# Kernel tuning notes

Measured on AMD Instinct MI355X. Metric: run time of the kernel, lower is better.

Reference implementation:

```python
import jax, jax.numpy as jnp
import numpy as np

N_POWER_SERIES = 8  # 'fixed' estimator, n_power_series=8, n_samples=4 (leading axis of v)


def _g_fn(x, W1, b1, W2, b2):
    # residual branch g(x): Linear -> ELU -> Linear (canonical i-ResNet block)
    return jax.nn.elu(x @ W1 + b1) @ W2 + b2


def setup_inputs() -> dict:
    key = jax.random.key(0)
    ks = jax.random.split(key, 4)
    B, D, H, S = 8192, 1024, 4096, 4
    x = jax.random.normal(ks[0], (B, D), jnp.float32)
    # scale weights so g is roughly contractive (Lipschitz < 1), as spectral norm enforces
    W1 = jax.random.normal(ks[1], (D, H), jnp.float32) * (0.5 / np.sqrt(D))
    b1 = jnp.zeros((H,), jnp.float32)
    W2 = jax.random.normal(ks[2], (H, D), jnp.float32) * (0.5 / np.sqrt(H))
    b2 = jnp.zeros((D,), jnp.float32)
    v = jax.random.normal(ks[3], (S, B, D), jnp.float32)  # Hutchinson probes
    log_df_dz = jnp.zeros((B,), jnp.float32)
    return {"x": x, "log_df_dz": log_df_dz, "W1": W1, "b1": b1, "W2": W2, "b2": b2, "v": v}


def reference(x, log_df_dz, W1, b1, W2, b2, v):
    g, vjp_fn = jax.vjp(lambda xx: _g_fn(xx, W1, b1, W2, b2), x)
    vjp = lambda w: vjp_fn(w)[0]  # w^T J, w: [B, D]

    w = v                      # [S, B, D]
    sum_diag = jnp.zeros(v.shape[:2], v.dtype)  # [S, B]
    for k in range(1, N_POWER_SERIES + 1):
        w = jax.vmap(vjp)(w)                        # v^T J^k
        inner = jnp.einsum('sbd,sbd->sb', w, v)     # Hutchinson tr(J^k) estimate
        sign = 1.0 if (k % 2 == 1) else -1.0
        sum_diag = sum_diag + sign * (inner / k)
    logdet = jnp.mean(sum_diag, axis=0)             # mean over samples -> [B]

    z = x + g
    return z, log_df_dz + logdet
```

## Files before the change

kernel.cpp:

```cpp
#include <hip/hip_runtime.h>
#include <hip/hip_bf16.h>

using bf16 = __hip_bfloat16;
typedef __attribute__((ext_vector_type(8))) short bf16x8;
typedef __attribute__((ext_vector_type(4))) float f32x4;

__device__ __forceinline__ float b2f(unsigned short u) {
  union { unsigned int i; float f; } x; x.i = ((unsigned int)u) << 16; return x.f;
}
__device__ __forceinline__ unsigned short f2b(float f) {
  __hip_bfloat16 h = __float2bfloat16(f);
  return *reinterpret_cast<unsigned short*>(&h);
}

__device__ __forceinline__ void load16_to_lds(const bf16* g, void* lds) {
  __builtin_amdgcn_global_load_lds((const __attribute__((address_space(1))) void*)g,
                                   (__attribute__((address_space(3))) void*)lds, 16, 0, 0);
}

#define FENCE() asm volatile("" ::: "memory")
#define BAR() do { FENCE(); __builtin_amdgcn_s_barrier(); FENCE(); } while (0)
#define SCHED_PIN() __builtin_amdgcn_sched_barrier(0)

__global__ void cast_f32_bf16(const float* __restrict__ in, bf16* __restrict__ out, size_t n) {
  size_t i0 = ((size_t)blockIdx.x * 256 + threadIdx.x) * 4;
  size_t stride = (size_t)gridDim.x * 256 * 4;
  for (size_t i = i0; i < n; i += stride) {
    float4 f = *(const float4*)(in + i);
    ushort4 o;
    o.x = f2b(f.x); o.y = f2b(f.y); o.z = f2b(f.z); o.w = f2b(f.w);
    *(ushort4*)(out + i) = o;
  }
}

__global__ void transpose_cast(const float* __restrict__ in, bf16* __restrict__ out, int R, int C) {
  __shared__ float tile[32][33];
  int tx = threadIdx.x & 31, ty = threadIdx.x >> 5;
  int r0 = blockIdx.y * 32, c0 = blockIdx.x * 32;
  #pragma unroll
  for (int i = 0; i < 32; i += 8)
    tile[ty + i][tx] = in[(size_t)(r0 + ty + i) * C + (c0 + tx)];
  __syncthreads();
  #pragma unroll
  for (int i = 0; i < 32; i += 8)
    out[(size_t)(c0 + ty + i) * R + (r0 + tx)] = __float2bfloat16(tile[tx][ty + i]);
}

template<int EPI>
__global__ __launch_bounds__(512, 2)
void gemm256(const bf16* __restrict__ A, const bf16* __restrict__ Bm,
             int M, int N, int K,
             bf16* __restrict__ OutB,
             const float* __restrict__ bias,
             const bf16* __restrict__ Ea) {
  __shared__ __align__(16) char pool[131072];
  char* Albs = pool;
  char* Blbs = pool + 65536;
  const int tid = threadIdx.x;
  const int l = tid & 63, w = tid >> 6;
  const int lane16 = l & 15, lh = l >> 4;
  const int wr = w >> 2, wc = w & 3;
  const int bm0 = blockIdx.y * 256, bn0 = blockIdx.x * 256;
  const int NT2 = K >> 7;

  auto stage = [&](const bf16* G, int grow0, int kbase, char* ldsbase) {
    #pragma unroll
    for (int r = 0; r < 2; ++r) {
      int p = (r * 512 + tid) * 16;
      int row = p >> 7, colb = p & 127;
      int cs = colb ^ ((row & 7) << 4);
      const bf16* g = G + (size_t)(grow0 + row) * K + kbase + (cs >> 1);
      load16_to_lds(g, ldsbase + (size_t)(r * 512 + w * 64) * 16);
    }
  };
  auto rd = [&](const char* base, int row, int colb) -> bf16x8 {
    return *(const bf16x8*)(base + row * 128 + (colb ^ ((row & 7) << 4)));
  };

  f32x4 acc[8][4] = {};
  bf16x8 a_r[4][2], b_r[4][2];

  #define RD_A(mq, buf) { _Pragma("unroll") for (int i = 0; i < 4; ++i) \
      _Pragma("unroll") for (int kk = 0; kk < 2; ++kk) \
      a_r[i][kk] = rd(Albs + (buf) * 32768, wr * 128 + (mq) * 64 + i * 16 + lane16, kk * 64 + lh * 16); }
  #define RD_B(buf) { _Pragma("unroll") for (int nf = 0; nf < 4; ++nf) \
      _Pragma("unroll") for (int kk = 0; kk < 2; ++kk) \
      b_r[nf][kk] = rd(Blbs + (buf) * 32768, wc * 64 + nf * 16 + lane16, kk * 64 + lh * 16); }
  #define MFMA_H(mq, n0) { __builtin_amdgcn_s_setprio(1); \
      _Pragma("unroll") for (int i = 0; i < 4; ++i) \
      _Pragma("unroll") for (int nn = 0; nn < 2; ++nn) \
      _Pragma("unroll") for (int kk = 0; kk < 2; ++kk) \
        acc[(mq)*4+i][(n0)+nn] = __builtin_amdgcn_mfma_f32_16x16x32_bf16( \
            a_r[i][kk], b_r[(n0)+nn][kk], acc[(mq)*4+i][(n0)+nn], 0, 0, 0); \
      __builtin_amdgcn_s_setprio(0); }
  #define PHASE(BODY_PRE, MFMA_CALL) { BODY_PRE; BAR(); SCHED_PIN(); MFMA_CALL; SCHED_PIN(); BAR(); }

  stage(Bm, bn0 + 0,   0,  Blbs + 0);
  stage(Bm, bn0 + 128, 0,  Blbs + 16384);
  stage(A,  bm0 + 0,   0,  Albs + 0);
  stage(A,  bm0 + 128, 0,  Albs + 16384);
  stage(Bm, bn0 + 0,   64, Blbs + 32768);
  stage(Bm, bn0 + 128, 64, Blbs + 32768 + 16384);
  stage(A,  bm0 + 0,   64, Albs + 32768);
  asm volatile("s_waitcnt vmcnt(6)" ::: "memory");
  SCHED_PIN();
  BAR();

  for (int t = 0; t < NT2; ++t) {
    const int k2 = (2 * t + 2) * 64, k3 = (2 * t + 3) * 64;
    const bool nl = (t < NT2 - 1);
    PHASE({ RD_B(0); RD_A(0, 0); stage(A, bm0 + 128, (2 * t + 1) * 64, Albs + 32768 + 16384); },
          MFMA_H(0, 0));
    PHASE({ if (nl) stage(Bm, bn0 + 0, k2, Blbs + 0); }, MFMA_H(0, 2));
    PHASE({ RD_A(1, 0); if (nl) stage(Bm, bn0 + 128, k2, Blbs + 16384); }, MFMA_H(1, 0));
    { if (nl) stage(A, bm0 + 0, k2, Albs + 0);
      BAR(); SCHED_PIN(); MFMA_H(1, 2); SCHED_PIN();
      if (nl) { asm volatile("s_waitcnt vmcnt(6)" ::: "memory"); }
      else    { asm volatile("s_waitcnt vmcnt(0)" ::: "memory"); }
      SCHED_PIN(); BAR(); }
    PHASE({ RD_B(1); RD_A(0, 1); if (nl) stage(A, bm0 + 128, k2, Albs + 16384); },
          MFMA_H(0, 0));
    PHASE({ if (nl) stage(Bm, bn0 + 0, k3, Blbs + 32768); }, MFMA_H(0, 2));
    PHASE({ RD_A(1, 1); if (nl) stage(Bm, bn0 + 128, k3, Blbs + 32768 + 16384); }, MFMA_H(1, 0));
    { if (nl) stage(A, bm0 + 0, k3, Albs + 32768);
      BAR(); SCHED_PIN(); MFMA_H(1, 2); SCHED_PIN();
      if (nl) { asm volatile("s_waitcnt vmcnt(6)" ::: "memory"); }
      SCHED_PIN(); BAR(); }
  }

  float* scr = (float*)(pool + w * 4352);
  const int row0 = bm0 + wr * 128, col0 = bn0 + wc * 64;
  const int erow = l >> 3, ecol = (l & 7) * 8;
  f32x4 bias0 = {}, bias1 = {};
  bf16x8 ea_pre[8][2];
  if (EPI == 0) {
    bias0 = *(const f32x4*)&bias[col0 + ecol];
    bias1 = *(const f32x4*)&bias[col0 + ecol + 4];
  } else {
    #pragma unroll
    for (int mf = 0; mf < 8; ++mf)
      #pragma unroll
      for (int p = 0; p < 2; ++p) {
        int gm = row0 + mf * 16 + p * 8 + erow;
        ea_pre[mf][p] = *(const bf16x8*)&Ea[(size_t)gm * N + col0 + ecol];
      }
  }
  SCHED_PIN();
  #pragma unroll
  for (int mf = 0; mf < 8; ++mf) {
    #pragma unroll
    for (int nf = 0; nf < 4; ++nf)
      #pragma unroll
      for (int q = 0; q < 4; ++q)
        scr[(lh * 4 + q) * 68 + nf * 16 + lane16] = acc[mf][nf][q];
    #pragma unroll
    for (int p = 0; p < 2; ++p) {
      int row = p * 8 + erow;
      const float* sp = &scr[row * 68 + ecol];
      f32x4 lo = *(const f32x4*)sp;
      f32x4 hi = *(const f32x4*)(sp + 4);
      int gm = row0 + mf * 16 + row;
      size_t idx = (size_t)gm * N + col0 + ecol;
      bf16x8 ov;
      if (EPI == 0) {
        #pragma unroll
        for (int j = 0; j < 8; ++j) {
          float fj = (j < 4) ? lo[j] : hi[j - 4];
          float bj = (j < 4) ? bias0[j] : bias1[j - 4];
          float hv = fj + bj;
          float a = hv > 0.f ? hv : expm1f(hv);
          ov[j] = (short)f2b(a);
        }
      } else {
        bf16x8 ea = ea_pre[mf][p];
        #pragma unroll
        for (int j = 0; j < 8; ++j) {
          float fj = (j < 4) ? lo[j] : hi[j - 4];
          float a = b2f((unsigned short)ea[j]);
          float e = a > 0.f ? 1.f : a + 1.f;
          ov[j] = (short)f2b(fj * e);
        }
      }
      *(bf16x8*)(&OutB[idx]) = ov;
    }
  }
  #undef RD_A
  #undef RD_B
  #undef MFMA_H
  #undef PHASE
}

template<int EPI>
__global__ __launch_bounds__(256)
void gemm_bt(const bf16* __restrict__ A, const bf16* __restrict__ Bm,
             int M, int N, int K,
             bf16* __restrict__ OutB, float* __restrict__ OutF,
             const float* __restrict__ bias, const float* __restrict__ Xadd,
             const float* __restrict__ Vf, float* __restrict__ sdg, float coef) {
  __shared__ __align__(16) char pool[4 * 4352];
  bf16* As = (bf16*)pool;
  bf16* Bs = (bf16*)(pool + 8192);
  const int tid = threadIdx.x;
  const int l = tid & 63, w = tid >> 6;
  const int wr = w >> 1, wc = w & 1;
  const int lane16 = l & 15, lh = l >> 4;
  const int bm0 = blockIdx.x * 128, bn0 = blockIdx.y * 128;

  f32x4 acc[4][4] = {};
  const int nk = K >> 5;
  for (int kt = 0; kt < nk; ++kt) {
    const size_t kbase = (size_t)kt * 32;
    #pragma unroll
    for (int i = 0; i < 2; ++i) {
      int c = i * 256 + w * 64 + l;
      int row = c >> 2;
      int cbs = ((((c & 3) << 4) ^ ((row & 6) << 3)) >> 1);
      const bf16* ga = A  + (size_t)(bm0 + row) * K + kbase + cbs;
      const bf16* gb = Bm + (size_t)(bn0 + row) * K + kbase + cbs;
      char* la = (char*)As + (size_t)(i * 256 + w * 64) * 16;
      char* lb = (char*)Bs + (size_t)(i * 256 + w * 64) * 16;
      load16_to_lds(ga, la);
      load16_to_lds(gb, lb);
    }
    __syncthreads();
    bf16x8 af[4], bfv[4];
    #pragma unroll
    for (int r = 0; r < 4; ++r) {
      int arow = wr * 64 + r * 16 + lane16;
      int aoff = (lh << 4) ^ ((arow & 6) << 3);
      af[r] = *(const bf16x8*)((const char*)As + arow * 64 + aoff);
    }
    #pragma unroll
    for (int c = 0; c < 4; ++c) {
      int brow = wc * 64 + c * 16 + lane16;
      int boff = (lh << 4) ^ ((brow & 6) << 3);
      bfv[c] = *(const bf16x8*)((const char*)Bs + brow * 64 + boff);
    }
    #pragma unroll
    for (int r = 0; r < 4; ++r)
      #pragma unroll
      for (int c = 0; c < 4; ++c)
        acc[r][c] = __builtin_amdgcn_mfma_f32_16x16x32_bf16(af[r], bfv[c], acc[r][c], 0, 0, 0);
    __syncthreads();
  }

  if (EPI == 1) {
    #pragma unroll
    for (int r = 0; r < 4; ++r) {
      int gm_base = bm0 + wr * 64 + r * 16 + lh * 4;
      #pragma unroll
      for (int c = 0; c < 4; ++c) {
        int gn = bn0 + wc * 64 + c * 16 + lane16;
        #pragma unroll
        for (int q = 0; q < 4; ++q) {
          size_t idx = (size_t)(gm_base + q) * N + gn;
          OutF[idx] = acc[r][c][q] + bias[gn] + Xadd[idx];
        }
      }
    }
  } else {
    float* scr = (float*)(pool + w * 4352);
    float* sdgslot = sdg + (size_t)(blockIdx.y * 2 + wc) * M;
    #pragma unroll
    for (int r = 0; r < 4; ++r) {
      #pragma unroll
      for (int c = 0; c < 4; ++c)
        #pragma unroll
        for (int q = 0; q < 4; ++q)
          scr[(lh * 4 + q) * 68 + c * 16 + lane16] = acc[r][c][q];
      #pragma unroll
      for (int p = 0; p < 2; ++p) {
        int row = p * 8 + (l >> 3);
        int c0 = (l & 7) * 8;
        const float* sp = &scr[row * 68 + c0];
        f32x4 lo = *(const f32x4*)sp;
        f32x4 hi = *(const f32x4*)(sp + 4);
        int gm = bm0 + wr * 64 + r * 16 + row;
        int gn = bn0 + wc * 64 + c0;
        size_t idx = (size_t)gm * N + gn;
        f32x4 v0 = *(const f32x4*)(Vf + idx);
        f32x4 v1 = *(const f32x4*)(Vf + idx + 4);
        float s = lo[0]*v0[0] + lo[1]*v0[1] + lo[2]*v0[2] + lo[3]*v0[3]
                + hi[0]*v1[0] + hi[1]*v1[1] + hi[2]*v1[2] + hi[3]*v1[3];
        s += __shfl_xor(s, 1); s += __shfl_xor(s, 2); s += __shfl_xor(s, 4);
        if ((l & 7) == 0) sdgslot[gm] += coef * s;
        if (OutB) {
          bf16x8 ov;
          #pragma unroll
          for (int j = 0; j < 8; ++j) {
            float fj = (j < 4) ? lo[j] : hi[j - 4];
            ov[j] = (short)f2b(fj);
          }
          *(bf16x8*)(&OutB[idx]) = ov;
        }
      }
      __syncthreads();
    }
  }
}

__global__ void finalize(const float* __restrict__ ldz, const float* __restrict__ sdp,
                         float* __restrict__ out, int B, int S) {
  int b = blockIdx.x * 256 + threadIdx.x;
  if (b >= B) return;
  float acc = 0.f;
  for (int s = 0; s < S; ++s)
    for (int p = 0; p < 16; ++p)
      acc += sdp[((size_t)s * 16 + p) * B + b];
  out[b] = ldz[b] + acc / (float)S;
}

extern "C" void kernel_launch(void* const* d_in, const int* in_sizes, int n_in,
                              void* d_out, int out_size, void* d_ws, size_t ws_size,
                              hipStream_t stream) {
  const int B = 8192, D = 1024, H = 4096, S = 4, NPS = 8;
  const float* x   = (const float*)d_in[0];
  const float* ldz = (const float*)d_in[1];
  const float* W1  = (const float*)d_in[2];
  const float* b1  = (const float*)d_in[3];
  const float* W2  = (const float*)d_in[4];
  const float* b2  = (const float*)d_in[5];
  const float* v   = (const float*)d_in[6];
  float* z_out  = (float*)d_out;
  float* ld_out = z_out + (size_t)B * D;

  char* ws = (char*)d_ws;
  size_t off = 0;
  auto alloc = [&](size_t bytes) {
    char* p = ws + off; off = (off + bytes + 255) & ~(size_t)255; return p;
  };
  float* sdgpart = (float*)alloc((size_t)S * 16 * B * 4);
  bf16* W1b  = (bf16*)alloc((size_t)D * H * 2);
  bf16* W2b  = (bf16*)alloc((size_t)D * H * 2);
  bf16* abuf = (bf16*)alloc((size_t)B * H * 2);
  bf16* wreg = (bf16*)alloc((size_t)B * D * 2);
  bf16* treg = (bf16*)alloc((size_t)B * H * 2);
  bf16* xb  = treg;
  bf16* W1T = (bf16*)((char*)treg + (size_t)16 * 1024 * 1024);
  bf16* W2T = (bf16*)((char*)treg + (size_t)24 * 1024 * 1024);
  (void)ws_size; (void)in_sizes; (void)n_in; (void)out_size;

  hipMemsetAsync(sdgpart, 0, (size_t)S * 16 * B * 4, stream);

  cast_f32_bf16<<<1024, 256, 0, stream>>>(x,  xb,  (size_t)B * D);
  cast_f32_bf16<<<1024, 256, 0, stream>>>(W1, W1b, (size_t)D * H);
  cast_f32_bf16<<<1024, 256, 0, stream>>>(W2, W2b, (size_t)D * H);
  transpose_cast<<<dim3(H / 32, D / 32), 256, 0, stream>>>(W1, W1T, D, H);
  transpose_cast<<<dim3(D / 32, H / 32), 256, 0, stream>>>(W2, W2T, H, D);

  gemm256<0><<<dim3(H / 256, B / 256), 512, 0, stream>>>(xb, W1T, B, H, D,
      abuf, b1, nullptr);
  gemm_bt<1><<<dim3(B / 128, D / 128), 256, 0, stream>>>(abuf, W2T, B, D, H,
      nullptr, z_out, b2, x, nullptr, nullptr, 0.f);

  for (int s = 0; s < S; ++s) {
    const float* vs = v + (size_t)s * B * D;
    cast_f32_bf16<<<1024, 256, 0, stream>>>(vs, wreg, (size_t)B * D);
    for (int k = 1; k <= NPS; ++k) {
      gemm256<2><<<dim3(H / 256, B / 256), 512, 0, stream>>>(wreg, W2b, B, H, D,
          treg, nullptr, abuf);
      float coef = ((k & 1) ? 1.f : -1.f) / (float)k;
      bf16* wout = (k < NPS) ? wreg : nullptr;
      gemm_bt<3><<<dim3(B / 128, D / 128), 256, 0, stream>>>(treg, W1b, B, D, H,
          wout, nullptr, nullptr, nullptr, vs, sdgpart + (size_t)s * 16 * B, coef);
    }
  }
  finalize<<<B / 256, 256, 0, stream>>>(ldz, sdgpart, ld_out, B, S);
}
```

Measured before the change: 5.933 ms.

## Shrink gemm_bt tile to 64x128 with per-wave column strips

Result: no change. 6.045 ms (+1.9%).

```diff
diff --git a/kernel.cpp b/kernel.cpp
--- a/kernel.cpp
+++ b/kernel.cpp
@@ -199,91 +199,92 @@
              const float* __restrict__ Vf, float* __restrict__ sdg, float coef) {
   __shared__ __align__(16) char pool[4 * 4352];
   bf16* As = (bf16*)pool;
-  bf16* Bs = (bf16*)(pool + 8192);
+  bf16* Bs = (bf16*)(pool + 4096);
   const int tid = threadIdx.x;
   const int l = tid & 63, w = tid >> 6;
-  const int wr = w >> 1, wc = w & 1;
   const int lane16 = l & 15, lh = l >> 4;
-  const int bm0 = blockIdx.x * 128, bn0 = blockIdx.y * 128;
-
-  f32x4 acc[4][4] = {};
+  const int bm0 = blockIdx.x * 64, bn0 = blockIdx.y * 128;
+
+  f32x4 acc[4][2] = {};
   const int nk = K >> 5;
   for (int kt = 0; kt < nk; ++kt) {
     const size_t kbase = (size_t)kt * 32;
+    {
+      int c = w * 64 + l;
+      int row = c >> 2;
+      int cbs = ((((c & 3) << 4) ^ ((row & 6) << 3)) >> 1);
+      const bf16* ga = A + (size_t)(bm0 + row) * K + kbase + cbs;
+      load16_to_lds(ga, (char*)As + (size_t)(w * 64) * 16);
+    }
     #pragma unroll
     for (int i = 0; i < 2; ++i) {
       int c = i * 256 + w * 64 + l;
       int row = c >> 2;
       int cbs = ((((c & 3) << 4) ^ ((row & 6) << 3)) >> 1);
-      const bf16* ga = A  + (size_t)(bm0 + row) * K + kbase + cbs;
       const bf16* gb = Bm + (size_t)(bn0 + row) * K + kbase + cbs;
-      char* la = (char*)As + (size_t)(i * 256 + w * 64) * 16;
-      char* lb = (char*)Bs + (size_t)(i * 256 + w * 64) * 16;
-      load16_to_lds(ga, la);
-      load16_to_lds(gb, lb);
+      load16_to_lds(gb, (char*)Bs + (size_t)(i * 256 + w * 64) * 16);
     }
     __syncthreads();
-    bf16x8 af[4], bfv[4];
+    bf16x8 af[4], bfv[2];
     #pragma unroll
     for (int r = 0; r < 4; ++r) {
-      int arow = wr * 64 + r * 16 + lane16;
+      int arow = r * 16 + lane16;
       int aoff = (lh << 4) ^ ((arow & 6) << 3);
       af[r] = *(const bf16x8*)((const char*)As + arow * 64 + aoff);
     }
     #pragma unroll
-    for (int c = 0; c < 4; ++c) {
-      int brow = wc * 64 + c * 16 + lane16;
+    for (int c2 = 0; c2 < 2; ++c2) {
+      int brow = w * 32 + c2 * 16 + lane16;
       int boff = (lh << 4) ^ ((brow & 6) << 3);
-      bfv[c] = *(const bf16x8*)((const char*)Bs + brow * 64 + boff);
+      bfv[c2] = *(const bf16x8*)((const char*)Bs + brow * 64 + boff);
     }
     #pragma unroll
     for (int r = 0; r < 4; ++r)
       #pragma unroll
-      for (int c = 0; c < 4; ++c)
-        acc[r][c] = __builtin_amdgcn_mfma_f32_16x16x32_bf16(af[r], bfv[c], acc[r][c], 0, 0, 0);
+      for (int c2 = 0; c2 < 2; ++c2)
+        acc[r][c2] = __builtin_amdgcn_mfma_f32_16x16x32_bf16(af[r], bfv[c2], acc[r][c2], 0, 0, 0);
     __syncthreads();
   }
 
   if (EPI == 1) {
     #pragma unroll
     for (int r = 0; r < 4; ++r) {
-      int gm_base = bm0 + wr * 64 + r * 16 + lh * 4;
-      #pragma unroll
-      for (int c = 0; c < 4; ++c) {
-        int gn = bn0 + wc * 64 + c * 16 + lane16;
+      int gm_base = bm0 + r * 16 + lh * 4;
+      #pragma unroll
+      for (int c2 = 0; c2 < 2; ++c2) {
+        int gn = bn0 + w * 32 + c2 * 16 + lane16;
         #pragma unroll
         for (int q = 0; q < 4; ++q) {
           size_t idx = (size_t)(gm_base + q) * N + gn;
-          OutF[idx] = acc[r][c][q] + bias[gn] + Xadd[idx];
+          OutF[idx] = acc[r][c2][q] + bias[gn] + Xadd[idx];
         }
       }
     }
   } else {
     float* scr = (float*)(pool + w * 4352);
-    float* sdgslot = sdg + (size_t)(blockIdx.y * 2 + wc) * M;
-    #pragma unroll
-    for (int r = 0; r < 4; ++r) {
-      #pragma unroll
-      for (int c = 0; c < 4; ++c)
+    float* sdgslot = sdg + (size_t)(blockIdx.y * 4 + w) * M;
+    #pragma unroll
+    for (int mf = 0; mf < 4; ++mf) {
+      #pragma unroll
+      for (int c2 = 0; c2 < 2; ++c2)
         #pragma unroll
         for (int q = 0; q < 4; ++q)
-          scr[(lh * 4 + q) * 68 + c * 16 + lane16] = acc[r][c][q];
-      #pragma unroll
-      for (int p = 0; p < 2; ++p) {
-        int row = p * 8 + (l >> 3);
-        int c0 = (l & 7) * 8;
-        const float* sp = &scr[row * 68 + c0];
+          scr[(lh * 4 + q) * 36 + c2 * 16 + lane16] = acc[mf][c2][q];
+      {
+        int row = l >> 2;
+        int c0 = (l & 3) * 8;
+        const float* sp = &scr[row * 36 + c0];
         f32x4 lo = *(const f32x4*)sp;
         f32x4 hi = *(const f32x4*)(sp + 4);
-        int gm = bm0 + wr * 64 + r * 16 + row;
-        int gn = bn0 + wc * 64 + c0;
+        int gm = bm0 + mf * 16 + row;
+        int gn = bn0 + w * 32 + c0;
         size_t idx = (size_t)gm * N + gn;
         f32x4 v0 = *(const f32x4*)(Vf + idx);
         f32x4 v1 = *(const f32x4*)(Vf + idx + 4);
         float s = lo[0]*v0[0] + lo[1]*v0[1] + lo[2]*v0[2] + lo[3]*v0[3]
                 + hi[0]*v1[0] + hi[1]*v1[1] + hi[2]*v1[2] + hi[3]*v1[3];
-        s += __shfl_xor(s, 1); s += __shfl_xor(s, 2); s += __shfl_xor(s, 4);
-        if ((l & 7) == 0) sdgslot[gm] += coef * s;
+        s += __shfl_xor(s, 1); s += __shfl_xor(s, 2);
+        if ((l & 3) == 0) sdgslot[gm] += coef * s;
         if (OutB) {
           bf16x8 ov;
           #pragma unroll
@@ -294,7 +295,7 @@
           *(bf16x8*)(&OutB[idx]) = ov;
         }
       }
-      __syncthreads();
+      FENCE();
     }
   }
 }
@@ -305,8 +306,8 @@
   if (b >= B) return;
   float acc = 0.f;
   for (int s = 0; s < S; ++s)
-    for (int p = 0; p < 16; ++p)
-      acc += sdp[((size_t)s * 16 + p) * B + b];
+    for (int p = 0; p < 32; ++p)
+      acc += sdp[((size_t)s * 32 + p) * B + b];
   out[b] = ldz[b] + acc / (float)S;
 }
 
@@ -329,7 +330,7 @@
   auto alloc = [&](size_t bytes) {
     char* p = ws + off; off = (off + bytes + 255) & ~(size_t)255; return p;
   };
-  float* sdgpart = (float*)alloc((size_t)S * 16 * B * 4);
+  float* sdgpart = (float*)alloc((size_t)S * 32 * B * 4);
   bf16* W1b  = (bf16*)alloc((size_t)D * H * 2);
   bf16* W2b  = (bf16*)alloc((size_t)D * H * 2);
   bf16* abuf = (bf16*)alloc((size_t)B * H * 2);
@@ -340,7 +341,7 @@
   bf16* W2T = (bf16*)((char*)treg + (size_t)24 * 1024 * 1024);
   (void)ws_size; (void)in_sizes; (void)n_in; (void)out_size;
 
-  hipMemsetAsync(sdgpart, 0, (size_t)S * 16 * B * 4, stream);
+  hipMemsetAsync(sdgpart, 0, (size_t)S * 32 * B * 4, stream);
 
   cast_f32_bf16<<<1024, 256, 0, stream>>>(x,  xb,  (size_t)B * D);
   cast_f32_bf16<<<1024, 256, 0, stream>>>(W1, W1b, (size_t)D * H);
@@ -350,7 +351,7 @@
 
   gemm256<0><<<dim3(H / 256, B / 256), 512, 0, stream>>>(xb, W1T, B, H, D,
       abuf, b1, nullptr);
-  gemm_bt<1><<<dim3(B / 128, D / 128), 256, 0, stream>>>(abuf, W2T, B, D, H,
+  gemm_bt<1><<<dim3(B / 64, D / 128), 256, 0, stream>>>(abuf, W2T, B, D, H,
       nullptr, z_out, b2, x, nullptr, nullptr, 0.f);
 
   for (int s = 0; s < S; ++s) {
@@ -361,8 +362,8 @@
           treg, nullptr, abuf);
       float coef = ((k & 1) ? 1.f : -1.f) / (float)k;
       bf16* wout = (k < NPS) ? wreg : nullptr;
-      gemm_bt<3><<<dim3(B / 128, D / 128), 256, 0, stream>>>(treg, W1b, B, D, H,
-          wout, nullptr, nullptr, nullptr, vs, sdgpart + (size_t)s * 16 * B, coef);
+      gemm_bt<3><<<dim3(B / 64, D / 128), 256, 0, stream>>>(treg, W1b, B, D, H,
+          wout, nullptr, nullptr, nullptr, vs, sdgpart + (size_t)s * 32 * B, coef);
     }
   }
   finalize<<<B / 256, 256, 0, stream>>>(ldz, sdgpart, ld_out, B, S);
```
